# Kernel tuning notes

Measured on AMD Instinct MI355X. Metric: run time of the kernel, lower is better.

The kernel has to match this reference:

```python
import jax, jax.numpy as jnp
import numpy as np

B = 32
HID = 2048
INNER = 4096       # expand_factor * hidden_size
NHEADS = 8
HEAD = INNER // NHEADS   # 512
KCONV = 4
CAP = 30.0         # gate_soft_cap
EPS = 1e-6
GN_EPS = 1e-5      # torch GroupNorm default eps


def setup_inputs() -> dict:
    key = jax.random.key(0)
    ks = jax.random.split(key, 12)
    s = 0.02
    return {
        "x": jax.random.normal(ks[0], (B, HID), jnp.float32),
        "conv_state": jax.random.normal(ks[1], (B, INNER, KCONV - 1), jnp.float32),
        "cell_state": jax.random.normal(ks[2], (B, NHEADS, HEAD, HEAD), jnp.float32) * 0.1,
        "norm_state": jax.random.normal(ks[3], (B, NHEADS, HEAD), jnp.float32) * 0.1,
        "max_state": jnp.zeros((B, NHEADS), jnp.float32),
        "rms_w": jnp.ones((HID,), jnp.float32),
        "Wx": jax.random.normal(ks[4], (INNER, HID), jnp.float32) * s,
        "Wg": jax.random.normal(ks[5], (INNER, HID), jnp.float32) * s,
        "Wqkv": jax.random.normal(ks[6], (3 * INNER, INNER), jnp.float32) * s,
        "conv_w": jax.random.normal(ks[7], (INNER, KCONV), jnp.float32) * s,
        "conv_b": jnp.zeros((INNER,), jnp.float32),
        "Wi": jax.random.normal(ks[8], (NHEADS, 3 * INNER), jnp.float32) * s,
        "bi": jnp.full((NHEADS,), -10.0, jnp.float32),
        "Wf": jax.random.normal(ks[9], (NHEADS, 3 * INNER), jnp.float32) * s,
        "bf": jnp.zeros((NHEADS,), jnp.float32),
        "gn_w": jnp.ones((INNER,), jnp.float32),
        "gn_b": jnp.zeros((INNER,), jnp.float32),
        "Wdown": jax.random.normal(ks[10], (HID, INNER), jnp.float32) * s,
        "skip_w": jnp.ones((INNER,), jnp.float32),
    }


def reference(x, conv_state, cell_state, norm_state, max_state,
              rms_w, Wx, Wg, Wqkv, conv_w, conv_b, Wi, bi, Wf, bf,
              gn_w, gn_b, Wdown, skip_w):
    skip = x
    # RMSNorm
    xn = x * jax.lax.rsqrt(jnp.mean(x * x, -1, keepdims=True) + EPS) * rms_w
    x_mlstm = xn @ Wx.T          # [B, INNER]
    x_gate = xn @ Wg.T           # [B, INNER]
    # depthwise causal conv over (state | current step)
    x_cat = jnp.concatenate([conv_state, x_mlstm[:, :, None]], -1)  # [B, INNER, K]
    x_conv = jnp.einsum('bck,ck->bc', x_cat, conv_w) + conv_b
    new_conv_state = x_cat[:, :, 1:]
    xmc = jax.nn.silu(x_conv)
    qkv = xmc @ Wqkv.T           # [B, 3*INNER] == cat(q,k,v)
    q, k, v = jnp.split(qkv, 3, axis=1)
    # gates (soft-capped)
    ig = CAP * jnp.tanh((qkv @ Wi.T + bi) / CAP)   # [B, H]
    fg = CAP * jnp.tanh((qkv @ Wf.T + bf) / CAP)
    qh = q.reshape(B, NHEADS, HEAD)
    kh = k.reshape(B, NHEADS, HEAD) / np.float32(np.sqrt(HEAD))
    vh = v.reshape(B, NHEADS, HEAD)
    log_f = jax.nn.log_sigmoid(fg)
    max_new = jnp.maximum(ig, max_state + log_f)
    i_gate = jnp.exp(ig - max_new)
    f_gate = jnp.exp(log_f + max_state - max_new)
    # outer-product state update
    cell_new = (f_gate[:, :, None, None] * cell_state
                + i_gate[:, :, None, None] * (kh[..., :, None] * vh[..., None, :]))
    norm_new = f_gate[..., None] * norm_state + i_gate[..., None] * kh
    # per-head readout
    numer = jnp.einsum('bhd,bhde->bhe', qh, cell_new)
    qn = jnp.sum(qh * norm_new, -1)                 # [B, H]
    denom = jnp.maximum(jnp.abs(qn), jnp.exp(-max_new)) + EPS
    out = numer / denom[..., None]                  # [B, H, d]
    # GroupNorm with num_groups = NHEADS over flattened channels
    mu = jnp.mean(out, -1, keepdims=True)
    var = jnp.mean((out - mu) ** 2, -1, keepdims=True)
    out = (out - mu) * jax.lax.rsqrt(var + GN_EPS)
    out = out.reshape(B, INNER) * gn_w + gn_b
    h = (out + skip_w * xmc) * jax.nn.silu(x_gate)
    y = h @ Wdown.T + skip
    return y, new_conv_state, cell_new, norm_new, max_new
```

## Files before the change

### kernel.cpp

```cpp
#include <hip/hip_runtime.h>
#include <hip/hip_bf16.h>

#define B_      32
#define HID_    2048
#define INNER_  4096
#define NH_     8
#define HEAD_   512
#define CAP_    30.0f

typedef short short8 __attribute__((ext_vector_type(8)));
typedef float f32x4 __attribute__((ext_vector_type(4)));

static __device__ __forceinline__ unsigned short f2bf(float f) {
    unsigned int u = __float_as_uint(f);
    u = (u + 0x7fffu + ((u >> 16) & 1u)) >> 16;
    return (unsigned short)u;
}

static __device__ __forceinline__ float sigm(float x) { return 1.0f / (1.0f + expf(-x)); }
static __device__ __forceinline__ float silu(float x) { return x * sigm(x); }

__global__ void k_rms(const float* __restrict__ x, const float* __restrict__ rms_w,
                      float* __restrict__ xn) {
    const int b = blockIdx.x, t = threadIdx.x;
    __shared__ float red[4];
    const float* xr = x + b * HID_;
    float s = 0.f;
    for (int i = t; i < HID_; i += 256) { float v = xr[i]; s += v * v; }
    for (int off = 32; off; off >>= 1) s += __shfl_down(s, off, 64);
    if ((t & 63) == 0) red[t >> 6] = s;
    __syncthreads();
    const float scale = rsqrtf((red[0] + red[1] + red[2] + red[3]) / (float)HID_ + 1e-6f);
    float* xo = xn + b * HID_;
    for (int i = t; i < HID_; i += 256) xo[i] = xr[i] * scale * rms_w[i];
}

__global__ void k_gemm(const float* __restrict__ A, const float* __restrict__ W,
                       float* __restrict__ C, int N, int K, int Kper) {
    __shared__ unsigned short Al[32][136];
    __shared__ unsigned short Wl[64][136];
    const int tid  = threadIdx.x;
    const int lane = tid & 63;
    const int wave = tid >> 6;
    const int quad = lane >> 4;
    const int l16  = lane & 15;
    const int oBlk = blockIdx.x * 64;
    const int k0s  = blockIdx.y * Kper;
    const int ntiles = Kper >> 7;

    f32x4 acc0 = {0.f, 0.f, 0.f, 0.f};
    f32x4 acc1 = {0.f, 0.f, 0.f, 0.f};

    for (int kt = 0; kt < ntiles; ++kt) {
        const int k0 = k0s + kt * 128;
        for (int i = tid; i < 1024; i += 256) {
            const int r = i >> 5, c = i & 31;
            const float4 f = *(const float4*)(A + r * K + k0 + c * 4);
            ushort4 u; u.x = f2bf(f.x); u.y = f2bf(f.y); u.z = f2bf(f.z); u.w = f2bf(f.w);
            *(ushort4*)&Al[r][c * 4] = u;
        }
        for (int i = tid; i < 2048; i += 256) {
            const int r = i >> 5, c = i & 31;
            const float4 f = *(const float4*)(W + (size_t)(oBlk + r) * K + k0 + c * 4);
            ushort4 u; u.x = f2bf(f.x); u.y = f2bf(f.y); u.z = f2bf(f.z); u.w = f2bf(f.w);
            *(ushort4*)&Wl[r][c * 4] = u;
        }
        __syncthreads();
        #pragma unroll
        for (int ks = 0; ks < 4; ++ks) {
            const int kk = ks * 32 + quad * 8;
            const short8 a0 = *(const short8*)&Al[l16][kk];
            const short8 a1 = *(const short8*)&Al[16 + l16][kk];
            const short8 wf = *(const short8*)&Wl[wave * 16 + l16][kk];
            acc0 = __builtin_amdgcn_mfma_f32_16x16x32_bf16(a0, wf, acc0, 0, 0, 0);
            acc1 = __builtin_amdgcn_mfma_f32_16x16x32_bf16(a1, wf, acc1, 0, 0, 0);
        }
        __syncthreads();
    }
    const int o = oBlk + wave * 16 + l16;
    #pragma unroll
    for (int r = 0; r < 4; ++r) {
        const int b0 = quad * 4 + r;
        atomicAdd(&C[(size_t)b0 * N + o], acc0[r]);
        atomicAdd(&C[(size_t)(16 + b0) * N + o], acc1[r]);
    }
}

__global__ void k_conv(const float* __restrict__ xm, const float* __restrict__ conv_state,
                       const float* __restrict__ conv_w, const float* __restrict__ conv_b,
                       float* __restrict__ xmc, float* __restrict__ ncs_out) {
    const int idx = blockIdx.x * 256 + threadIdx.x;
    if (idx >= B_ * INNER_) return;
    const int c = idx & (INNER_ - 1);
    const float* cs = conv_state + (size_t)idx * 3;
    const float c0 = cs[0], c1 = cs[1], c2 = cs[2];
    const float xv = xm[idx];
    const float* w = conv_w + c * 4;
    const float conv = c0 * w[0] + c1 * w[1] + c2 * w[2] + xv * w[3] + conv_b[c];
    xmc[idx] = silu(conv);
    float* no = ncs_out + (size_t)idx * 3;
    no[0] = c1; no[1] = c2; no[2] = xv;
}

__global__ void k_gates(const float* __restrict__ qkv, const float* __restrict__ Wi,
                        const float* __restrict__ bi, const float* __restrict__ Wf,
                        const float* __restrict__ bfv, const float* __restrict__ max_state,
                        float* __restrict__ i_gate, float* __restrict__ f_gate,
                        float* __restrict__ max_new) {
    const int bh = blockIdx.x, b = bh >> 3, h = bh & 7, t = threadIdx.x;
    const float* q  = qkv + (size_t)b * (3 * INNER_);
    const float* wi = Wi + (size_t)h * (3 * INNER_);
    const float* wf = Wf + (size_t)h * (3 * INNER_);
    float si = 0.f, sf = 0.f;
    for (int j = t; j < 3 * INNER_; j += 256) {
        const float v = q[j];
        si += v * wi[j];
        sf += v * wf[j];
    }
    __shared__ float r1[4], r2[4];
    for (int off = 32; off; off >>= 1) {
        si += __shfl_down(si, off, 64);
        sf += __shfl_down(sf, off, 64);
    }
    if ((t & 63) == 0) { r1[t >> 6] = si; r2[t >> 6] = sf; }
    __syncthreads();
    if (t == 0) {
        float ig = r1[0] + r1[1] + r1[2] + r1[3] + bi[h];
        float fg = r2[0] + r2[1] + r2[2] + r2[3] + bfv[h];
        ig = CAP_ * tanhf(ig / CAP_);
        fg = CAP_ * tanhf(fg / CAP_);
        const float logf_ = (fg >= 0.f) ? -log1pf(expf(-fg)) : (fg - log1pf(expf(fg)));
        const float ms = max_state[bh];
        const float mn = fmaxf(ig, ms + logf_);
        max_new[bh] = mn;
        i_gate[bh] = expf(ig - mn);
        f_gate[bh] = expf(logf_ + ms - mn);
    }
}

__global__ void k_cell(const float* __restrict__ qkv, const float* __restrict__ i_gate,
                       const float* __restrict__ f_gate, const float* __restrict__ max_new,
                       const float* __restrict__ cell_state, const float* __restrict__ norm_state,
                       const float* __restrict__ gn_w, const float* __restrict__ gn_b,
                       const float* __restrict__ skip_w, const float* __restrict__ xmc,
                       const float* __restrict__ x_gate,
                       float* __restrict__ cell_out, float* __restrict__ norm_out,
                       float* __restrict__ h_out) {
    const int bh = blockIdx.x, b = bh >> 3, h = bh & 7, t = threadIdx.x;
    __shared__ float q_l[HEAD_], ik_l[HEAD_], nsum[HEAD_];
    __shared__ float redA[4], redB[4];
    const float i_g = i_gate[bh], f_g = f_gate[bh], mx = max_new[bh];
    const float rs = 0.044194173824159216f;
    const float* qr = qkv + (size_t)b * (3 * INNER_) + h * HEAD_;
    const float* kr = qr + INNER_;
    const float* vr = qr + 2 * INNER_;
    const float* ns = norm_state + (size_t)bh * HEAD_;

    float qn = 0.f;
    for (int d = t; d < HEAD_; d += 256) {
        const float qv = qr[d];
        const float ik = i_g * (kr[d] * rs);
        q_l[d] = qv; ik_l[d] = ik;
        const float nn = f_g * ns[d] + ik;
        norm_out[(size_t)bh * HEAD_ + d] = nn;
        qn += qv * nn;
    }
    for (int off = 32; off; off >>= 1) qn += __shfl_down(qn, off, 64);
    if ((t & 63) == 0) redA[t >> 6] = qn;
    __syncthreads();
    qn = redA[0] + redA[1] + redA[2] + redA[3];
    const float denom = fmaxf(fabsf(qn), expf(-mx)) + 1e-6f;

    const int half = t >> 7;
    const int e0 = (t & 127) * 4;
    const float4 v4 = *(const float4*)(vr + e0);
    float4 num = {0.f, 0.f, 0.f, 0.f};
    const float* cin = cell_state + (size_t)bh * (HEAD_ * HEAD_);
    float* cout = cell_out + (size_t)bh * (HEAD_ * HEAD_);
    const int d0 = half * 256;
    for (int d = d0; d < d0 + 256; ++d) {
        const float4 c4 = *(const float4*)(cin + (size_t)d * HEAD_ + e0);
        const float ik = ik_l[d], qv = q_l[d];
        float4 cn;
        cn.x = f_g * c4.x + ik * v4.x;
        cn.y = f_g * c4.y + ik * v4.y;
        cn.z = f_g * c4.z + ik * v4.z;
        cn.w = f_g * c4.w + ik * v4.w;
        *(float4*)(cout + (size_t)d * HEAD_ + e0) = cn;
        num.x += qv * cn.x; num.y += qv * cn.y; num.z += qv * cn.z; num.w += qv * cn.w;
    }
    __syncthreads();
    if (half == 0) { nsum[e0] = num.x; nsum[e0+1] = num.y; nsum[e0+2] = num.z; nsum[e0+3] = num.w; }
    __syncthreads();
    if (half == 1) { nsum[e0] += num.x; nsum[e0+1] += num.y; nsum[e0+2] += num.z; nsum[e0+3] += num.w; }
    __syncthreads();

    float s = 0.f, s2 = 0.f;
    for (int e = t; e < HEAD_; e += 256) {
        const float o = nsum[e] / denom;
        s += o; s2 += o * o;
    }
    for (int off = 32; off; off >>= 1) {
        s  += __shfl_down(s, off, 64);
        s2 += __shfl_down(s2, off, 64);
    }
    if ((t & 63) == 0) { redA[t >> 6] = s; redB[t >> 6] = s2; }
    __syncthreads();
    const float mu  = (redA[0] + redA[1] + redA[2] + redA[3]) / (float)HEAD_;
    const float ex2 = (redB[0] + redB[1] + redB[2] + redB[3]) / (float)HEAD_;
    const float inv = rsqrtf(fmaxf(ex2 - mu * mu, 0.f) + 1e-5f);

    for (int e = t; e < HEAD_; e += 256) {
        const int i = h * HEAD_ + e;
        const float og = (nsum[e] / denom - mu) * inv * gn_w[i] + gn_b[i];
        const float xg = x_gate[(size_t)b * INNER_ + i];
        const float hv = (og + skip_w[i] * xmc[(size_t)b * INNER_ + i]) * silu(xg);
        h_out[(size_t)b * INNER_ + i] = hv;
    }
}

extern "C" void kernel_launch(void* const* d_in, const int* in_sizes, int n_in,
                              void* d_out, int out_size, void* d_ws, size_t ws_size,
                              hipStream_t stream) {
    const float* x          = (const float*)d_in[0];
    const float* conv_state = (const float*)d_in[1];
    const float* cell_state = (const float*)d_in[2];
    const float* norm_state = (const float*)d_in[3];
    const float* max_state  = (const float*)d_in[4];
    const float* rms_w      = (const float*)d_in[5];
    const float* Wx         = (const float*)d_in[6];
    const float* Wg         = (const float*)d_in[7];
    const float* Wqkv       = (const float*)d_in[8];
    const float* conv_w     = (const float*)d_in[9];
    const float* conv_b     = (const float*)d_in[10];
    const float* Wi         = (const float*)d_in[11];
    const float* bi         = (const float*)d_in[12];
    const float* Wf         = (const float*)d_in[13];
    const float* bfv        = (const float*)d_in[14];
    const float* gn_w       = (const float*)d_in[15];
    const float* gn_b       = (const float*)d_in[16];
    const float* Wdown      = (const float*)d_in[17];
    const float* skip_w     = (const float*)d_in[18];

    float* out = (float*)d_out;
    float* y_out    = out;
    float* ncs_out  = y_out + B_ * HID_;
    float* cell_out = ncs_out + (size_t)B_ * INNER_ * 3;
    float* norm_out = cell_out + (size_t)B_ * NH_ * HEAD_ * HEAD_;
    float* max_out  = norm_out + (size_t)B_ * NH_ * HEAD_;

    float* w = (float*)d_ws;
    float* xn      = w;
    float* xmc     = xn + B_ * HID_;
    float* h_ws    = xmc + B_ * INNER_;
    float* i_g_ws  = h_ws + B_ * INNER_;
    float* f_g_ws  = i_g_ws + B_ * NH_;
    float* x_mlstm = f_g_ws + B_ * NH_;
    float* x_gate  = x_mlstm + B_ * INNER_;
    float* qkv     = x_gate + B_ * INNER_;

    hipMemsetAsync(x_mlstm, 0, (size_t)(2 * B_ * INNER_ + B_ * 3 * INNER_) * 4, stream);
    hipMemcpyAsync(y_out, x, (size_t)B_ * HID_ * 4, hipMemcpyDeviceToDevice, stream);

    k_rms<<<B_, 256, 0, stream>>>(x, rms_w, xn);

    k_gemm<<<dim3(INNER_ / 64, 8), 256, 0, stream>>>(xn, Wx, x_mlstm, INNER_, HID_, HID_ / 8);
    k_gemm<<<dim3(INNER_ / 64, 8), 256, 0, stream>>>(xn, Wg, x_gate, INNER_, HID_, HID_ / 8);

    k_conv<<<(B_ * INNER_) / 256, 256, 0, stream>>>(x_mlstm, conv_state, conv_w, conv_b,
                                                    xmc, ncs_out);

    k_gemm<<<dim3(3 * INNER_ / 64, 4), 256, 0, stream>>>(xmc, Wqkv, qkv,
                                                         3 * INNER_, INNER_, INNER_ / 4);

    k_gates<<<B_ * NH_, 256, 0, stream>>>(qkv, Wi, bi, Wf, bfv, max_state,
                                          i_g_ws, f_g_ws, max_out);

    k_cell<<<B_ * NH_, 256, 0, stream>>>(qkv, i_g_ws, f_g_ws, max_out, cell_state, norm_state,
                                         gn_w, gn_b, skip_w, xmc, x_gate,
                                         cell_out, norm_out, h_ws);

    k_gemm<<<dim3(HID_ / 64, 8), 256, 0, stream>>>(h_ws, Wdown, y_out, HID_, INNER_, INNER_ / 8);
}
```

Measured before the change: 739.3 us.

## Split mLSTM cell update across row chunks and move norm/denom into gates kernel

The cell-state update kernel is split so each (batch, head) is handled by 8 blocks over 64-row chunks, with partial readout numerators combined via atomicAdd into a zeroed workspace. The norm-state update and denominator are moved into the gates kernel, and GroupNorm plus gating move into a new epilogue kernel. Split-K factors for the QKV and down-projection GEMMs are raised to spread more blocks across CUs. This aims to raise occupancy of the memory-bound 268MB cell-state pass, at the cost of an extra launch, float atomics, and more atomic traffic in the GEMMs.

```diff
diff --git a/kernel.cpp b/kernel.cpp
--- a/kernel.cpp
+++ b/kernel.cpp
@@ -7,6 +7,7 @@
 #define NH_     8
 #define HEAD_   512
 #define CAP_    30.0f
+#define DCH_    64
 
 typedef short short8 __attribute__((ext_vector_type(8)));
 typedef float f32x4 __attribute__((ext_vector_type(4)));
@@ -35,7 +36,8 @@
     for (int i = t; i < HID_; i += 256) xo[i] = xr[i] * scale * rms_w[i];
 }
 
-__global__ void k_gemm(const float* __restrict__ A, const float* __restrict__ W,
+__global__ __launch_bounds__(256) void k_gemm(const float* __restrict__ A,
+                       const float* __restrict__ W,
                        float* __restrict__ C, int N, int K, int Kper) {
     __shared__ unsigned short Al[32][136];
     __shared__ unsigned short Wl[64][136];
@@ -105,8 +107,10 @@
 __global__ void k_gates(const float* __restrict__ qkv, const float* __restrict__ Wi,
                         const float* __restrict__ bi, const float* __restrict__ Wf,
                         const float* __restrict__ bfv, const float* __restrict__ max_state,
-                        float* __restrict__ i_gate, float* __restrict__ f_gate,
-                        float* __restrict__ max_new) {
+                        const float* __restrict__ norm_state,
+                        float* __restrict__ ig_ws, float* __restrict__ fg_ws,
+                        float* __restrict__ max_new, float* __restrict__ norm_out,
+                        float* __restrict__ denom_ws) {
     const int bh = blockIdx.x, b = bh >> 3, h = bh & 7, t = threadIdx.x;
     const float* q  = qkv + (size_t)b * (3 * INNER_);
     const float* wi = Wi + (size_t)h * (3 * INNER_);
@@ -117,7 +121,7 @@
         si += v * wi[j];
         sf += v * wf[j];
     }
-    __shared__ float r1[4], r2[4];
+    __shared__ float r1[4], r2[4], sc[3];
     for (int off = 32; off; off >>= 1) {
         si += __shfl_down(si, off, 64);
         sf += __shfl_down(sf, off, 64);
@@ -132,72 +136,98 @@
         const float logf_ = (fg >= 0.f) ? -log1pf(expf(-fg)) : (fg - log1pf(expf(fg)));
         const float ms = max_state[bh];
         const float mn = fmaxf(ig, ms + logf_);
-        max_new[bh] = mn;
-        i_gate[bh] = expf(ig - mn);
-        f_gate[bh] = expf(logf_ + ms - mn);
-    }
-}
-
-__global__ void k_cell(const float* __restrict__ qkv, const float* __restrict__ i_gate,
-                       const float* __restrict__ f_gate, const float* __restrict__ max_new,
-                       const float* __restrict__ cell_state, const float* __restrict__ norm_state,
-                       const float* __restrict__ gn_w, const float* __restrict__ gn_b,
-                       const float* __restrict__ skip_w, const float* __restrict__ xmc,
-                       const float* __restrict__ x_gate,
-                       float* __restrict__ cell_out, float* __restrict__ norm_out,
-                       float* __restrict__ h_out) {
-    const int bh = blockIdx.x, b = bh >> 3, h = bh & 7, t = threadIdx.x;
-    __shared__ float q_l[HEAD_], ik_l[HEAD_], nsum[HEAD_];
-    __shared__ float redA[4], redB[4];
-    const float i_g = i_gate[bh], f_g = f_gate[bh], mx = max_new[bh];
+        const float i_g = expf(ig - mn);
+        const float f_g = expf(logf_ + ms - mn);
+        max_new[bh] = mn; ig_ws[bh] = i_g; fg_ws[bh] = f_g;
+        sc[0] = i_g; sc[1] = f_g; sc[2] = mn;
+    }
+    __syncthreads();
+    const float i_g = sc[0], f_g = sc[1], mx = sc[2];
+    const float rs = 0.044194173824159216f;
+    const float* qr = q + h * HEAD_;
+    const float* kr = qr + INNER_;
+    const float* ns = norm_state + (size_t)bh * HEAD_;
+    float qn = 0.f;
+    for (int d = t; d < HEAD_; d += 256) {
+        const float qv = qr[d];
+        const float nn = f_g * ns[d] + i_g * (kr[d] * rs);
+        norm_out[(size_t)bh * HEAD_ + d] = nn;
+        qn += qv * nn;
+    }
+    for (int off = 32; off; off >>= 1) qn += __shfl_down(qn, off, 64);
+    if ((t & 63) == 0) r1[t >> 6] = qn;
+    __syncthreads();
+    if (t == 0) {
+        const float q_total = r1[0] + r1[1] + r1[2] + r1[3];
+        denom_ws[bh] = fmaxf(fabsf(q_total), expf(-mx)) + 1e-6f;
+    }
+}
+
+__global__ __launch_bounds__(256) void k_cell(const float* __restrict__ qkv,
+                       const float* __restrict__ ig_ws, const float* __restrict__ fg_ws,
+                       const float* __restrict__ cell_state,
+                       float* __restrict__ cell_out, float* __restrict__ numer_ws) {
+    const int blk = blockIdx.x;
+    const int bh = blk >> 3, chunk = blk & 7;
+    const int b = bh >> 3, h = bh & 7, t = threadIdx.x;
+    const int d0 = chunk * DCH_;
+    __shared__ float q_l[DCH_], ik_l[DCH_];
+    __shared__ float nred[HEAD_];
+    const float i_g = ig_ws[bh], f_g = fg_ws[bh];
     const float rs = 0.044194173824159216f;
     const float* qr = qkv + (size_t)b * (3 * INNER_) + h * HEAD_;
     const float* kr = qr + INNER_;
     const float* vr = qr + 2 * INNER_;
-    const float* ns = norm_state + (size_t)bh * HEAD_;
-
-    float qn = 0.f;
-    for (int d = t; d < HEAD_; d += 256) {
-        const float qv = qr[d];
-        const float ik = i_g * (kr[d] * rs);
-        q_l[d] = qv; ik_l[d] = ik;
-        const float nn = f_g * ns[d] + ik;
-        norm_out[(size_t)bh * HEAD_ + d] = nn;
-        qn += qv * nn;
-    }
-    for (int off = 32; off; off >>= 1) qn += __shfl_down(qn, off, 64);
-    if ((t & 63) == 0) redA[t >> 6] = qn;
-    __syncthreads();
-    qn = redA[0] + redA[1] + redA[2] + redA[3];
-    const float denom = fmaxf(fabsf(qn), expf(-mx)) + 1e-6f;
-
+    if (t < DCH_) {
+        q_l[t]  = qr[d0 + t];
+        ik_l[t] = i_g * (kr[d0 + t] * rs);
+    }
+    __syncthreads();
     const int half = t >> 7;
-    const int e0 = (t & 127) * 4;
-    const float4 v4 = *(const float4*)(vr + e0);
+    const int col  = (t & 127) * 4;
+    const float4 v4 = *(const float4*)(vr + col);
+    const float* pin  = cell_state + (size_t)bh * HEAD_ * HEAD_ + (size_t)(d0 + half) * HEAD_ + col;
+    float*       pout = cell_out   + (size_t)bh * HEAD_ * HEAD_ + (size_t)(d0 + half) * HEAD_ + col;
     float4 num = {0.f, 0.f, 0.f, 0.f};
-    const float* cin = cell_state + (size_t)bh * (HEAD_ * HEAD_);
-    float* cout = cell_out + (size_t)bh * (HEAD_ * HEAD_);
-    const int d0 = half * 256;
-    for (int d = d0; d < d0 + 256; ++d) {
-        const float4 c4 = *(const float4*)(cin + (size_t)d * HEAD_ + e0);
+    #pragma unroll 4
+    for (int it = 0; it < DCH_ / 2; ++it) {
+        const int d = it * 2 + half;
+        const float4 c4 = *(const float4*)pin;
         const float ik = ik_l[d], qv = q_l[d];
         float4 cn;
         cn.x = f_g * c4.x + ik * v4.x;
         cn.y = f_g * c4.y + ik * v4.y;
         cn.z = f_g * c4.z + ik * v4.z;
         cn.w = f_g * c4.w + ik * v4.w;
-        *(float4*)(cout + (size_t)d * HEAD_ + e0) = cn;
+        *(float4*)pout = cn;
         num.x += qv * cn.x; num.y += qv * cn.y; num.z += qv * cn.z; num.w += qv * cn.w;
-    }
-    __syncthreads();
-    if (half == 0) { nsum[e0] = num.x; nsum[e0+1] = num.y; nsum[e0+2] = num.z; nsum[e0+3] = num.w; }
-    __syncthreads();
-    if (half == 1) { nsum[e0] += num.x; nsum[e0+1] += num.y; nsum[e0+2] += num.z; nsum[e0+3] += num.w; }
-    __syncthreads();
-
+        pin  += 2 * HEAD_;
+        pout += 2 * HEAD_;
+    }
+    if (half == 0) {
+        nred[col] = num.x; nred[col+1] = num.y; nred[col+2] = num.z; nred[col+3] = num.w;
+    }
+    __syncthreads();
+    if (half == 1) {
+        float* nw = numer_ws + (size_t)bh * HEAD_;
+        atomicAdd(&nw[col],     nred[col]     + num.x);
+        atomicAdd(&nw[col + 1], nred[col + 1] + num.y);
+        atomicAdd(&nw[col + 2], nred[col + 2] + num.z);
+        atomicAdd(&nw[col + 3], nred[col + 3] + num.w);
+    }
+}
+
+__global__ void k_epi(const float* __restrict__ numer_ws, const float* __restrict__ denom_ws,
+                      const float* __restrict__ gn_w, const float* __restrict__ gn_b,
+                      const float* __restrict__ skip_w, const float* __restrict__ xmc,
+                      const float* __restrict__ x_gate, float* __restrict__ h_out) {
+    const int bh = blockIdx.x, b = bh >> 3, h = bh & 7, t = threadIdx.x;
+    __shared__ float redA[4], redB[4];
+    const float denom = denom_ws[bh];
+    const float* nu = numer_ws + (size_t)bh * HEAD_;
     float s = 0.f, s2 = 0.f;
     for (int e = t; e < HEAD_; e += 256) {
-        const float o = nsum[e] / denom;
+        const float o = nu[e] / denom;
         s += o; s2 += o * o;
     }
     for (int off = 32; off; off >>= 1) {
@@ -209,10 +239,9 @@
     const float mu  = (redA[0] + redA[1] + redA[2] + redA[3]) / (float)HEAD_;
     const float ex2 = (redB[0] + redB[1] + redB[2] + redB[3]) / (float)HEAD_;
     const float inv = rsqrtf(fmaxf(ex2 - mu * mu, 0.f) + 1e-5f);
-
     for (int e = t; e < HEAD_; e += 256) {
         const int i = h * HEAD_ + e;
-        const float og = (nsum[e] / denom - mu) * inv * gn_w[i] + gn_b[i];
+        const float og = (nu[e] / denom - mu) * inv * gn_w[i] + gn_b[i];
         const float xg = x_gate[(size_t)b * INNER_ + i];
         const float hv = (og + skip_w[i] * xmc[(size_t)b * INNER_ + i]) * silu(xg);
         h_out[(size_t)b * INNER_ + i] = hv;
@@ -250,16 +279,19 @@
     float* max_out  = norm_out + (size_t)B_ * NH_ * HEAD_;
 
     float* w = (float*)d_ws;
-    float* xn      = w;
-    float* xmc     = xn + B_ * HID_;
-    float* h_ws    = xmc + B_ * INNER_;
-    float* i_g_ws  = h_ws + B_ * INNER_;
-    float* f_g_ws  = i_g_ws + B_ * NH_;
-    float* x_mlstm = f_g_ws + B_ * NH_;
-    float* x_gate  = x_mlstm + B_ * INNER_;
-    float* qkv     = x_gate + B_ * INNER_;
-
-    hipMemsetAsync(x_mlstm, 0, (size_t)(2 * B_ * INNER_ + B_ * 3 * INNER_) * 4, stream);
+    float* xn       = w;
+    float* xmc      = xn + B_ * HID_;
+    float* h_ws     = xmc + B_ * INNER_;
+    float* ig_ws    = h_ws + B_ * INNER_;
+    float* fg_ws    = ig_ws + B_ * NH_;
+    float* denom_ws = fg_ws + B_ * NH_;
+    float* x_mlstm  = denom_ws + B_ * NH_;
+    float* x_gate   = x_mlstm + B_ * INNER_;
+    float* qkv      = x_gate + B_ * INNER_;
+    float* numer_ws = qkv + B_ * 3 * INNER_;
+
+    hipMemsetAsync(x_mlstm, 0,
+                   (size_t)(2 * B_ * INNER_ + B_ * 3 * INNER_ + B_ * NH_ * HEAD_) * 4, stream);
     hipMemcpyAsync(y_out, x, (size_t)B_ * HID_ * 4, hipMemcpyDeviceToDevice, stream);
 
     k_rms<<<B_, 256, 0, stream>>>(x, rms_w, xn);
@@ -270,15 +302,17 @@
     k_conv<<<(B_ * INNER_) / 256, 256, 0, stream>>>(x_mlstm, conv_state, conv_w, conv_b,
                                                     xmc, ncs_out);
 
-    k_gemm<<<dim3(3 * INNER_ / 64, 4), 256, 0, stream>>>(xmc, Wqkv, qkv,
-                                                         3 * INNER_, INNER_, INNER_ / 4);
-
-    k_gates<<<B_ * NH_, 256, 0, stream>>>(qkv, Wi, bi, Wf, bfv, max_state,
-                                          i_g_ws, f_g_ws, max_out);
-
-    k_cell<<<B_ * NH_, 256, 0, stream>>>(qkv, i_g_ws, f_g_ws, max_out, cell_state, norm_state,
-                                         gn_w, gn_b, skip_w, xmc, x_gate,
-                                         cell_out, norm_out, h_ws);
-
-    k_gemm<<<dim3(HID_ / 64, 8), 256, 0, stream>>>(h_ws, Wdown, y_out, HID_, INNER_, INNER_ / 8);
-}
+    k_gemm<<<dim3(3 * INNER_ / 64, 8), 256, 0, stream>>>(xmc, Wqkv, qkv,
+                                                         3 * INNER_, INNER_, INNER_ / 8);
+
+    k_gates<<<B_ * NH_, 256, 0, stream>>>(qkv, Wi, bi, Wf, bfv, max_state, norm_state,
+                                          ig_ws, fg_ws, max_out, norm_out, denom_ws);
+
+    k_cell<<<B_ * NH_ * 8, 256, 0, stream>>>(qkv, ig_ws, fg_ws, cell_state,
+                                             cell_out, numer_ws);
+
+    k_epi<<<B_ * NH_, 256, 0, stream>>>(numer_ws, denom_ws, gn_w, gn_b, skip_w,
+                                        xmc, x_gate, h_ws);
+
+    k_gemm<<<dim3(HID_ / 64, 16), 256, 0, stream>>>(h_ws, Wdown, y_out, HID_, INNER_, INNER_ / 16);
+}
```

After: 718.8 us. 1.03x faster.
